# Kernel optimization log

Hardware: AMD Instinct MI355X
Metric: run time of the kernel (lower is better)

The kernel has to match this reference:

```python
import jax, jax.numpy as jnp
import numpy as np

N = 50000
E = 800000
IN_DIM, HID, HEADS, OUT = 128, 32, 8, 64
NEG_SLOPE = 0.2
EPS = 1e-16


def setup_inputs() -> dict:
    key = jax.random.key(0)
    ks = jax.random.split(key, 10)
    return {
        "x": jax.random.normal(ks[0], (N, IN_DIM), dtype=jnp.float32),
        "edge_index": jax.random.randint(ks[1], (2, E), 0, N, dtype=jnp.int64)
        if jax.config.jax_enable_x64 else jax.random.randint(ks[1], (2, E), 0, N, dtype=jnp.int32),
        "W1": jax.random.normal(ks[2], (HEADS * HID, IN_DIM), dtype=jnp.float32) * 0.1,
        "att_src1": jax.random.normal(ks[3], (HEADS, HID), dtype=jnp.float32) * 0.1,
        "att_dst1": jax.random.normal(ks[4], (HEADS, HID), dtype=jnp.float32) * 0.1,
        "b1": jnp.zeros((HEADS * HID,), dtype=jnp.float32),
        "W2": jax.random.normal(ks[5], (OUT, HEADS * HID), dtype=jnp.float32) * 0.1,
        "att_src2": jax.random.normal(ks[6], (1, OUT), dtype=jnp.float32) * 0.1,
        "att_dst2": jax.random.normal(ks[7], (1, OUT), dtype=jnp.float32) * 0.1,
        "b2": jnp.zeros((OUT,), dtype=jnp.float32),
    }


def _gat_conv(x, src, dst, W, att_src, att_dst, bias, heads, out_dim, concat, n_nodes):
    # x: [N, F_in]; W: [heads*out_dim, F_in]; att_*: [heads, out_dim]
    h = (x @ W.T).reshape(n_nodes, heads, out_dim)      # [N, H, D]
    a_src = jnp.einsum('nhd,hd->nh', h, att_src)         # [N, H]
    a_dst = jnp.einsum('nhd,hd->nh', h, att_dst)
    alpha = jax.nn.leaky_relu(a_src[src] + a_dst[dst], NEG_SLOPE)  # [E, H]
    # segment softmax over edges grouped by destination node
    m = jax.ops.segment_max(alpha, dst, num_segments=n_nodes)
    alpha = jnp.exp(alpha - m[dst])
    s = jax.ops.segment_sum(alpha, dst, num_segments=n_nodes)
    alpha = alpha / (s[dst] + EPS)
    msg = h[src] * alpha[:, :, None]                     # [E, H, D]
    out = jax.ops.segment_sum(msg, dst, num_segments=n_nodes)  # [N, H, D]
    if concat:
        out = out.reshape(n_nodes, heads * out_dim)
    else:
        out = out.mean(axis=1)
    return out + bias


def reference(x, edge_index, W1, att_src1, att_dst1, b1, W2, att_src2, att_dst2, b2):
    n = x.shape[0]
    loop = jnp.arange(n, dtype=edge_index.dtype)
    src = jnp.concatenate([edge_index[0], loop])  # PyG add_self_loops=True
    dst = jnp.concatenate([edge_index[1], loop])
    h = _gat_conv(x, src, dst, W1, att_src1, att_dst1, b1, HEADS, HID, True, n)
    h = jax.nn.relu(h)
    out = _gat_conv(h, src, dst, W2, att_src2, att_dst2, b2, 1, OUT, False, n)
    return out
```

## Files before the change

kernel.cpp:

```cpp
#include <hip/hip_runtime.h>
#include <hip/hip_fp16.h>

#define NN 50000
#define EE 800000
#define ET (EE + NN)
#define IND 128
#define F1 256
#define H1 8
#define D1 32
#define F2 64
#define NEG 0.2f
#define EPSV 1e-16f

#define MG2 391
#define SCB ((ET + 2047) / 2048)
#define BCAP 64

typedef _Float16 half8_t __attribute__((ext_vector_type(8)));
typedef float floatx4 __attribute__((ext_vector_type(4)));

#define W1N4 (256 * 128 / 4)
#define W2N4 (64 * 256 / 4)
__global__ void k_cvtW(const float* __restrict__ w1, const float* __restrict__ w2,
                       __half* __restrict__ w1p, __half* __restrict__ w2h) {
  int i = blockIdx.x * blockDim.x + threadIdx.x;
  if (i < W1N4) {
    float4 v = *(const float4*)(w1 + (size_t)i * 4);
    int col = i >> 5;
    int kb = (i * 4) & 127;
    int by = col >> 7, t = (col >> 4) & 7, ar = col & 15;
    int kk = kb >> 5, ag = (kb >> 3) & 3, j = kb & 7;
    int fid = (by * 8 + t) * 4 + kk;
    int lane = ag * 16 + ar;
    __half2 p0 = __floats2half2_rn(v.x, v.y);
    __half2 p1 = __floats2half2_rn(v.z, v.w);
    float2 st;
    *(__half2*)&st.x = p0;
    *(__half2*)&st.y = p1;
    *(float2*)(w1p + fid * 512 + lane * 8 + j) = st;
    return;
  }
  i -= W1N4;
  if (i >= W2N4) return;
  float4 v = *(const float4*)(w2 + (size_t)i * 4);
  __half2 p0 = __floats2half2_rn(v.x, v.y);
  __half2 p1 = __floats2half2_rn(v.z, v.w);
  float2 st;
  *(__half2*)&st.x = p0;
  *(__half2*)&st.y = p1;
  *(float2*)(w2h + (size_t)i * 4) = st;
}

__global__ __launch_bounds__(256) void k_scg1(const int* __restrict__ ei,
    int* __restrict__ deg, unsigned short* __restrict__ bkt,
    const float* __restrict__ A, const __half* __restrict__ Bp,
    __half* __restrict__ Ch) {
  if (blockIdx.x >= 2 * MG2) {
    int base = (blockIdx.x - 2 * MG2) * 2048 + threadIdx.x * 8;
    if (base >= ET) return;
    if (base + 8 <= EE) {
      int4 s0 = *(const int4*)(ei + base);
      int4 s1 = *(const int4*)(ei + base + 4);
      int4 d0 = *(const int4*)(ei + EE + base);
      int4 d1 = *(const int4*)(ei + EE + base + 4);
      int s[8] = {s0.x, s0.y, s0.z, s0.w, s1.x, s1.y, s1.z, s1.w};
      int d[8] = {d0.x, d0.y, d0.z, d0.w, d1.x, d1.y, d1.z, d1.w};
#pragma unroll
      for (int j = 0; j < 8; ++j) {
        int pos = atomicAdd(&deg[d[j]], 1);
        if (pos < BCAP) bkt[(d[j] << 6) + pos] = (unsigned short)s[j];
      }
    } else {
      for (int j = 0; j < 8; ++j) {
        int e = base + j;
        if (e >= ET) break;
        int ss, dd;
        if (e < EE) { ss = ei[e]; dd = ei[EE + e]; }
        else        { ss = e - EE; dd = ss; }
        int pos = atomicAdd(&deg[dd], 1);
        if (pos < BCAP) bkt[(dd << 6) + pos] = (unsigned short)ss;
      }
    }
    return;
  }
  int bx = blockIdx.x % MG2, by = blockIdx.x / MG2;
  int tid = threadIdx.x;
  int wv = tid >> 6, lane = tid & 63;
  int m0 = bx * 128 + wv * 16;
  int ar = lane & 15, ag = lane >> 4;
  int r0 = m0 + ar;       if (r0 >= NN) r0 = NN - 1;
  int r1 = m0 + 64 + ar;  if (r1 >= NN) r1 = NN - 1;
  const float* A0 = A + (size_t)r0 * IND + ag * 8;
  const float* A1 = A + (size_t)r1 * IND + ag * 8;
  floatx4 acc[2][8];
#pragma unroll
  for (int rt = 0; rt < 2; ++rt)
#pragma unroll
    for (int t = 0; t < 8; ++t) acc[rt][t] = (floatx4){0.f, 0.f, 0.f, 0.f};
#pragma unroll
  for (int kk = 0; kk < 4; ++kk) {
    int k0 = kk * 32;
    float4 a00 = *(const float4*)(A0 + k0);
    float4 a01 = *(const float4*)(A0 + k0 + 4);
    float4 a10 = *(const float4*)(A1 + k0);
    float4 a11 = *(const float4*)(A1 + k0 + 4);
    half8_t af0, af1;
    af0[0] = (_Float16)a00.x; af0[1] = (_Float16)a00.y;
    af0[2] = (_Float16)a00.z; af0[3] = (_Float16)a00.w;
    af0[4] = (_Float16)a01.x; af0[5] = (_Float16)a01.y;
    af0[6] = (_Float16)a01.z; af0[7] = (_Float16)a01.w;
    af1[0] = (_Float16)a10.x; af1[1] = (_Float16)a10.y;
    af1[2] = (_Float16)a10.z; af1[3] = (_Float16)a10.w;
    af1[4] = (_Float16)a11.x; af1[5] = (_Float16)a11.y;
    af1[6] = (_Float16)a11.z; af1[7] = (_Float16)a11.w;
#pragma unroll
    for (int t = 0; t < 8; ++t) {
      int fid = (by * 8 + t) * 4 + kk;
      half8_t bf = *(const half8_t*)(Bp + fid * 512 + lane * 8);
      acc[0][t] = __builtin_amdgcn_mfma_f32_16x16x32_f16(af0, bf, acc[0][t], 0, 0, 0);
      acc[1][t] = __builtin_amdgcn_mfma_f32_16x16x32_f16(af1, bf, acc[1][t], 0, 0, 0);
    }
  }
#pragma unroll
  for (int rt = 0; rt < 2; ++rt)
#pragma unroll
    for (int t = 0; t < 8; ++t) {
      int col = by * 128 + t * 16 + ar;
#pragma unroll
      for (int r = 0; r < 4; ++r) {
        int m = m0 + rt * 64 + ag * 4 + r;
        if (m < NN) Ch[(size_t)m * F1 + col] = __float2half(acc[rt][t][r]);
      }
    }
}

template<int H, int D>
__global__ void k_att2(const __half* __restrict__ h, const float* __restrict__ atts,
                       const float* __restrict__ attd, float* __restrict__ as_,
                       float* __restrict__ ad_) {
  const int F = H * D;
  const int CPR = F / 8;
  const int NPW = 64 / CPR;
  const int CPH = D / 8;
  int lane = threadIdx.x & 63;
  int wv = threadIdx.x >> 6;
  int n = blockIdx.x * (4 * NPW) + wv * NPW + lane / CPR;
  if (n >= NN) return;
  int c = lane % CPR;
  int head = c / CPH;
  int within = c % CPH;
  half8_t f = *(const half8_t*)(h + (size_t)n * F + c * 8);
  float s_ = 0.f, d_ = 0.f;
#pragma unroll
  for (int j = 0; j < 8; ++j) {
    float fv = (float)f[j];
    s_ += fv * atts[head * D + within * 8 + j];
    d_ += fv * attd[head * D + within * 8 + j];
  }
#pragma unroll
  for (int m = 1; m < CPH; m <<= 1) {
    s_ += __shfl_xor(s_, m);
    d_ += __shfl_xor(d_, m);
  }
  if (within == 0) {
    as_[n * H + head] = s_;
    ad_[n * H + head] = d_;
  }
}

__global__ __launch_bounds__(256) void k_agg1(const int* __restrict__ deg,
    const unsigned short* __restrict__ bkt, const __half* __restrict__ feat,
    const float* __restrict__ as_, const float* __restrict__ ad_,
    const float* __restrict__ bias, __half* __restrict__ outh) {
  int wid = threadIdx.x >> 6;
  int lane = threadIdx.x & 63;
  int d = blockIdx.x * 4 + wid;
  if (d >= NN) return;
  const int b = lane >> 5;
  const int q = lane & 31;
  const int h = q >> 2;
  const int sw = lane >> 3;
  const int hw = lane & 7;
  const char* fb = (const char*)feat;
  float adw = ad_[d * 8 + hw];
  float acc[8] = {};
  float wsacc = 0.f;
  int p0 = d << 6;
  int dg = deg[d];
  int p1 = p0 + dg;
  int nfull = dg >> 3;
  int p = p0;
  for (int it = 0; it < nfull; ++it, p += 8) {
    int sW = bkt[p + sw];
    float t = as_[sW * 8 + hw] + adw;
    t = (t > 0.f) ? t : NEG * t;
    float w = __expf(t);
    wsacc += w;
    int wbits = __float_as_int(w);
#pragma unroll
    for (int i = 0; i < 4; ++i) {
      int slot = 2 * i + b;
      int se = __builtin_amdgcn_ds_bpermute(slot * 32, sW);
      float wv = __int_as_float(
          __builtin_amdgcn_ds_bpermute((slot * 8 + h) * 4, wbits));
      half8_t f = *(const half8_t*)(fb + ((se << 9) | (q << 4)));
#pragma unroll
      for (int j = 0; j < 8; ++j) acc[j] = fmaf(wv, (float)f[j], acc[j]);
    }
  }
  if (p < p1) {
    int pw = p + sw;
    bool v = pw < p1;
    int sW = bkt[v ? pw : (p1 - 1)];
    float t = as_[sW * 8 + hw] + adw;
    t = (t > 0.f) ? t : NEG * t;
    float w = v ? __expf(t) : 0.f;
    wsacc += w;
    int wbits = __float_as_int(w);
#pragma unroll
    for (int i = 0; i < 4; ++i) {
      int slot = 2 * i + b;
      int se = __builtin_amdgcn_ds_bpermute(slot * 32, sW);
      float wv = __int_as_float(
          __builtin_amdgcn_ds_bpermute((slot * 8 + h) * 4, wbits));
      half8_t f = *(const half8_t*)(fb + ((se << 9) | (q << 4)));
#pragma unroll
      for (int j = 0; j < 8; ++j) acc[j] = fmaf(wv, (float)f[j], acc[j]);
    }
  }
  wsacc += __shfl_xor(wsacc, 8);
  wsacc += __shfl_xor(wsacc, 16);
  wsacc += __shfl_xor(wsacc, 32);
  float wst = __int_as_float(
      __builtin_amdgcn_ds_bpermute(h * 4, __float_as_int(wsacc)));
#pragma unroll
  for (int j = 0; j < 8; ++j) acc[j] += __shfl_xor(acc[j], 32);
  if (b == 0) {
    float inv = 1.f / (wst + EPSV);
    __half2 packs[4];
#pragma unroll
    for (int j = 0; j < 8; j += 2) {
      float o0 = fmaxf(fmaf(acc[j], inv, 0.f) + bias[q * 8 + j], 0.f);
      float o1 = fmaxf(fmaf(acc[j + 1], inv, 0.f) + bias[q * 8 + j + 1], 0.f);
      packs[j >> 1] = __floats2half2_rn(o0, o1);
    }
    *(float4*)(outh + (size_t)d * 256 + q * 8) = *(float4*)packs;
  }
}

__global__ __launch_bounds__(256) void k_g2att(const __half* __restrict__ A,
    const __half* __restrict__ Bh, __half* __restrict__ Ch,
    const float* __restrict__ as2w, const float* __restrict__ ad2w,
    float* __restrict__ as2, float* __restrict__ ad2) {
  __shared__ __half Bs[64][256 + 8];
  int tid = threadIdx.x;
  const float4* src = (const float4*)Bh;
  for (int i = tid; i < 64 * 256 / 8; i += 256) {
    int row = i / 32, kc = i % 32;
    *(float4*)&Bs[row][kc * 8] = src[i];
  }
  __syncthreads();
  int wv = tid >> 6, lane = tid & 63;
  int m0 = blockIdx.x * 128 + wv * 16;
  int ar = lane & 15, ag = lane >> 4;
  int r0 = m0 + ar;       if (r0 >= NN) r0 = NN - 1;
  int r1 = m0 + 64 + ar;  if (r1 >= NN) r1 = NN - 1;
  const __half* A0 = A + (size_t)r0 * F1 + ag * 8;
  const __half* A1 = A + (size_t)r1 * F1 + ag * 8;
  floatx4 acc[2][4];
#pragma unroll
  for (int rt = 0; rt < 2; ++rt)
#pragma unroll
    for (int t = 0; t < 4; ++t) acc[rt][t] = (floatx4){0.f, 0.f, 0.f, 0.f};
#pragma unroll
  for (int k0 = 0; k0 < F1; k0 += 32) {
    half8_t af0 = *(const half8_t*)(A0 + k0);
    half8_t af1 = *(const half8_t*)(A1 + k0);
#pragma unroll
    for (int t = 0; t < 4; ++t) {
      half8_t bf = *(const half8_t*)&Bs[t * 16 + ar][k0 + ag * 8];
      acc[0][t] = __builtin_amdgcn_mfma_f32_16x16x32_f16(af0, bf, acc[0][t], 0, 0, 0);
      acc[1][t] = __builtin_amdgcn_mfma_f32_16x16x32_f16(af1, bf, acc[1][t], 0, 0, 0);
    }
  }
  float sp[2][4] = {}, dp[2][4] = {};
#pragma unroll
  for (int t = 0; t < 4; ++t) {
    int col = t * 16 + ar;
    float ws = as2w[col], wd = ad2w[col];
#pragma unroll
    for (int rt = 0; rt < 2; ++rt)
#pragma unroll
      for (int r = 0; r < 4; ++r) {
        int m = m0 + rt * 64 + ag * 4 + r;
        if (m < NN) Ch[(size_t)m * F2 + col] = __float2half(acc[rt][t][r]);
        sp[rt][r] = fmaf(acc[rt][t][r], ws, sp[rt][r]);
        dp[rt][r] = fmaf(acc[rt][t][r], wd, dp[rt][r]);
      }
  }
#pragma unroll
  for (int msk = 1; msk < 16; msk <<= 1)
#pragma unroll
    for (int rt = 0; rt < 2; ++rt)
#pragma unroll
      for (int r = 0; r < 4; ++r) {
        sp[rt][r] += __shfl_xor(sp[rt][r], msk);
        dp[rt][r] += __shfl_xor(dp[rt][r], msk);
      }
  if (ar == 0) {
#pragma unroll
    for (int rt = 0; rt < 2; ++rt)
#pragma unroll
      for (int r = 0; r < 4; ++r) {
        int m = m0 + rt * 64 + ag * 4 + r;
        if (m < NN) { as2[m] = sp[rt][r]; ad2[m] = dp[rt][r]; }
      }
  }
}

__global__ __launch_bounds__(256) void k_agg2(const int* __restrict__ deg,
    const unsigned short* __restrict__ bkt, const __half* __restrict__ feat,
    const float* __restrict__ as_, const float* __restrict__ ad_,
    const float* __restrict__ bias, float* __restrict__ out) {
  int wid = threadIdx.x >> 6;
  int lane = threadIdx.x & 63;
  int d = blockIdx.x * 4 + wid;
  if (d >= NN) return;
  const int b = lane >> 3;
  const int q = lane & 7;
  const char* fb = (const char*)feat;
  float adv = ad_[d];
  float acc[8] = {};
  float ws = 0.f;
  int p0 = d << 6;
  int dg = deg[d];
  int p1 = p0 + dg;
  int nfull = dg >> 3;
  int p = p0;
  for (int it = 0; it < nfull; ++it, p += 8) {
    int se = bkt[p + b];
    float t = as_[se] + adv;
    t = (t > 0.f) ? t : NEG * t;
    float w = __expf(t);
    ws += w;
    half8_t f = *(const half8_t*)(fb + ((se << 7) | (q << 4)));
#pragma unroll
    for (int j = 0; j < 8; ++j) acc[j] = fmaf(w, (float)f[j], acc[j]);
  }
  if (p < p1) {
    int pe = p + b;
    bool v = pe < p1;
    int se = bkt[v ? pe : (p1 - 1)];
    float t = as_[se] + adv;
    t = (t > 0.f) ? t : NEG * t;
    float w = v ? __expf(t) : 0.f;
    ws += w;
    half8_t f = *(const half8_t*)(fb + ((se << 7) | (q << 4)));
#pragma unroll
    for (int j = 0; j < 8; ++j) acc[j] = fmaf(w, (float)f[j], acc[j]);
  }
  ws += __shfl_xor(ws, 8);
  ws += __shfl_xor(ws, 16);
  ws += __shfl_xor(ws, 32);
#pragma unroll
  for (int j = 0; j < 8; ++j) {
    acc[j] += __shfl_xor(acc[j], 8);
    acc[j] += __shfl_xor(acc[j], 16);
    acc[j] += __shfl_xor(acc[j], 32);
  }
  if (b == 0) {
    float inv = 1.f / (ws + EPSV);
    float o[8];
#pragma unroll
    for (int j = 0; j < 8; ++j) o[j] = acc[j] * inv + bias[q * 8 + j];
    *(float4*)(out + (size_t)d * 64 + q * 8) = *(float4*)&o[0];
    *(float4*)(out + (size_t)d * 64 + q * 8 + 4) = *(float4*)&o[4];
  }
}

extern "C" void kernel_launch(void* const* d_in, const int* in_sizes, int n_in,
                              void* d_out, int out_size, void* d_ws, size_t ws_size,
                              hipStream_t stream) {
  const float* x    = (const float*)d_in[0];
  const int*   ei   = (const int*)d_in[1];
  const float* W1   = (const float*)d_in[2];
  const float* as1w = (const float*)d_in[3];
  const float* ad1w = (const float*)d_in[4];
  const float* b1   = (const float*)d_in[5];
  const float* W2   = (const float*)d_in[6];
  const float* as2w = (const float*)d_in[7];
  const float* ad2w = (const float*)d_in[8];
  const float* b2   = (const float*)d_in[9];
  float* out = (float*)d_out;

  char* W = (char*)d_ws;
  __half* h1h = (__half*)W; W += (size_t)NN * 256 * 2;
  __half* h2h = (__half*)W; W += (size_t)NN * 256 * 2;
  __half* hmh = (__half*)W; W += (size_t)NN * 64 * 2;
  __half* W1p = (__half*)W; W += 256 * 128 * 2;
  __half* W2h = (__half*)W; W += 64 * 256 * 2;
  float* as1 = (float*)W; W += (size_t)NN * 8 * 4;
  float* ad1 = (float*)W; W += (size_t)NN * 8 * 4;
  float* as2 = (float*)W; W += (size_t)NN * 4;
  float* ad2 = (float*)W; W += (size_t)NN * 4;
  int* deg    = (int*)W;  W += (size_t)NN * 4;
  unsigned short* bkt = (unsigned short*)W; W += (size_t)NN * BCAP * 2;

  hipMemsetAsync(deg, 0, NN * sizeof(int), stream);

  k_cvtW<<<(W1N4 + W2N4 + 255) / 256, 256, 0, stream>>>(W1, W2, W1p, W2h);
  k_scg1<<<2 * MG2 + SCB, 256, 0, stream>>>(ei, deg, bkt, x, W1p, h1h);
  k_att2<H1, D1><<<(NN + 7) / 8, 256, 0, stream>>>(h1h, as1w, ad1w, as1, ad1);
  k_agg1<<<(NN + 3) / 4, 256, 0, stream>>>(deg, bkt, h1h, as1, ad1, b1, h2h);
  k_g2att<<<MG2, 256, 0, stream>>>(h2h, W2h, hmh, as2w, ad2w, as2, ad2);
  k_agg2<<<(NN + 3) / 4, 256, 0, stream>>>(deg, bkt, hmh, as2, ad2, b2, out);
}
```

Baseline: 176.9 us.

## Pad degree counters to 64B, reorder scatter blocks first, batch atomics

Each destination's degree counter now sits on its own 64-byte line (stride 16 ints), which spreads atomic contention across lines and cache channels. The edge-scatter blocks are dispatched before the GEMM blocks in the fused kernel and handle 4 edges per thread instead of 8, with all four atomics issued before the bucket stores. In exchange the counter array grows 16x, so the memset is larger and the aggregation kernels' degree reads are no longer contiguous.

```diff
diff --git a/kernel.cpp b/kernel.cpp
--- a/kernel.cpp
+++ b/kernel.cpp
@@ -13,7 +13,7 @@
 #define EPSV 1e-16f
 
 #define MG2 391
-#define SCB ((ET + 2047) / 2048)
+#define SCB ((ET + 1023) / 1024)
 #define BCAP 64
 
 typedef _Float16 half8_t __attribute__((ext_vector_type(8)));
@@ -52,38 +52,38 @@
 }
 
 __global__ __launch_bounds__(256) void k_scg1(const int* __restrict__ ei,
-    int* __restrict__ deg, unsigned short* __restrict__ bkt,
+    int* __restrict__ deg16, unsigned short* __restrict__ bkt,
     const float* __restrict__ A, const __half* __restrict__ Bp,
     __half* __restrict__ Ch) {
-  if (blockIdx.x >= 2 * MG2) {
-    int base = (blockIdx.x - 2 * MG2) * 2048 + threadIdx.x * 8;
+  if (blockIdx.x < SCB) {
+    int base = blockIdx.x * 1024 + threadIdx.x * 4;
     if (base >= ET) return;
-    if (base + 8 <= EE) {
-      int4 s0 = *(const int4*)(ei + base);
-      int4 s1 = *(const int4*)(ei + base + 4);
-      int4 d0 = *(const int4*)(ei + EE + base);
-      int4 d1 = *(const int4*)(ei + EE + base + 4);
-      int s[8] = {s0.x, s0.y, s0.z, s0.w, s1.x, s1.y, s1.z, s1.w};
-      int d[8] = {d0.x, d0.y, d0.z, d0.w, d1.x, d1.y, d1.z, d1.w};
-#pragma unroll
-      for (int j = 0; j < 8; ++j) {
-        int pos = atomicAdd(&deg[d[j]], 1);
-        if (pos < BCAP) bkt[(d[j] << 6) + pos] = (unsigned short)s[j];
-      }
+    int s[4], d[4], pos[4];
+    if (base + 4 <= EE) {
+      int4 sv = *(const int4*)(ei + base);
+      int4 dv = *(const int4*)(ei + EE + base);
+      s[0] = sv.x; s[1] = sv.y; s[2] = sv.z; s[3] = sv.w;
+      d[0] = dv.x; d[1] = dv.y; d[2] = dv.z; d[3] = dv.w;
+#pragma unroll
+      for (int j = 0; j < 4; ++j) pos[j] = atomicAdd(&deg16[d[j] << 4], 1);
+#pragma unroll
+      for (int j = 0; j < 4; ++j)
+        if (pos[j] < BCAP) bkt[(d[j] << 6) + pos[j]] = (unsigned short)s[j];
     } else {
-      for (int j = 0; j < 8; ++j) {
+      for (int j = 0; j < 4; ++j) {
         int e = base + j;
         if (e >= ET) break;
         int ss, dd;
         if (e < EE) { ss = ei[e]; dd = ei[EE + e]; }
         else        { ss = e - EE; dd = ss; }
-        int pos = atomicAdd(&deg[dd], 1);
-        if (pos < BCAP) bkt[(dd << 6) + pos] = (unsigned short)ss;
+        int p = atomicAdd(&deg16[dd << 4], 1);
+        if (p < BCAP) bkt[(dd << 6) + p] = (unsigned short)ss;
       }
     }
     return;
   }
-  int bx = blockIdx.x % MG2, by = blockIdx.x / MG2;
+  int b = blockIdx.x - SCB;
+  int bx = b % MG2, by = b / MG2;
   int tid = threadIdx.x;
   int wv = tid >> 6, lane = tid & 63;
   int m0 = bx * 128 + wv * 16;
@@ -168,7 +168,7 @@
   }
 }
 
-__global__ __launch_bounds__(256) void k_agg1(const int* __restrict__ deg,
+__global__ __launch_bounds__(256) void k_agg1(const int* __restrict__ deg16,
     const unsigned short* __restrict__ bkt, const __half* __restrict__ feat,
     const float* __restrict__ as_, const float* __restrict__ ad_,
     const float* __restrict__ bias, __half* __restrict__ outh) {
@@ -186,7 +186,7 @@
   float acc[8] = {};
   float wsacc = 0.f;
   int p0 = d << 6;
-  int dg = deg[d];
+  int dg = deg16[d << 4];
   int p1 = p0 + dg;
   int nfull = dg >> 3;
   int p = p0;
@@ -318,7 +318,7 @@
   }
 }
 
-__global__ __launch_bounds__(256) void k_agg2(const int* __restrict__ deg,
+__global__ __launch_bounds__(256) void k_agg2(const int* __restrict__ deg16,
     const unsigned short* __restrict__ bkt, const __half* __restrict__ feat,
     const float* __restrict__ as_, const float* __restrict__ ad_,
     const float* __restrict__ bias, float* __restrict__ out) {
@@ -333,7 +333,7 @@
   float acc[8] = {};
   float ws = 0.f;
   int p0 = d << 6;
-  int dg = deg[d];
+  int dg = deg16[d << 4];
   int p1 = p0 + dg;
   int nfull = dg >> 3;
   int p = p0;
@@ -403,15 +403,15 @@
   float* ad1 = (float*)W; W += (size_t)NN * 8 * 4;
   float* as2 = (float*)W; W += (size_t)NN * 4;
   float* ad2 = (float*)W; W += (size_t)NN * 4;
-  int* deg    = (int*)W;  W += (size_t)NN * 4;
+  int* deg16  = (int*)W;  W += (size_t)NN * 16 * 4;
   unsigned short* bkt = (unsigned short*)W; W += (size_t)NN * BCAP * 2;
 
-  hipMemsetAsync(deg, 0, NN * sizeof(int), stream);
+  hipMemsetAsync(deg16, 0, (size_t)NN * 16 * sizeof(int), stream);
 
   k_cvtW<<<(W1N4 + W2N4 + 255) / 256, 256, 0, stream>>>(W1, W2, W1p, W2h);
-  k_scg1<<<2 * MG2 + SCB, 256, 0, stream>>>(ei, deg, bkt, x, W1p, h1h);
+  k_scg1<<<SCB + 2 * MG2, 256, 0, stream>>>(ei, deg16, bkt, x, W1p, h1h);
   k_att2<H1, D1><<<(NN + 7) / 8, 256, 0, stream>>>(h1h, as1w, ad1w, as1, ad1);
-  k_agg1<<<(NN + 3) / 4, 256, 0, stream>>>(deg, bkt, h1h, as1, ad1, b1, h2h);
+  k_agg1<<<(NN + 3) / 4, 256, 0, stream>>>(deg16, bkt, h1h, as1, ad1, b1, h2h);
   k_g2att<<<MG2, 256, 0, stream>>>(h2h, W2h, hmh, as2w, ad2w, as2, ad2);
-  k_agg2<<<(NN + 3) / 4, 256, 0, stream>>>(deg, bkt, hmh, as2, ad2, b2, out);
-}
+  k_agg2<<<(NN + 3) / 4, 256, 0, stream>>>(deg16, bkt, hmh, as2, ad2, b2, out);
+}
```

After: 195.7 us. 10.6% more time.
